# Kernel tuning notes

Measured on AMD Instinct MI355X. Metric: run time of the kernel, lower is better.

The kernel has to match this reference:

```python
import jax, jax.numpy as jnp
import numpy as np

PAD = 128  # attention_limit; window = 2*PAD+1 = 257


def setup_inputs() -> dict:
    key = jax.random.key(0)
    ks = jax.random.split(key, 8)
    B, S, E = 4, 4096, 512
    x = jax.random.normal(ks[0], (B, S, E), dtype=jnp.float32)
    mask = jax.random.randint(ks[1], (B, S, 1), 0, 2, dtype=jnp.int32)
    s = 1.0 / np.sqrt(E)
    Wq = jax.random.normal(ks[2], (E, E), dtype=jnp.float32) * s
    bq = jax.random.normal(ks[3], (E,), dtype=jnp.float32) * 0.01
    Wk = jax.random.normal(ks[4], (E, E), dtype=jnp.float32) * s
    bk = jax.random.normal(ks[5], (E,), dtype=jnp.float32) * 0.01
    Wv = jax.random.normal(ks[6], (E, E), dtype=jnp.float32) * s
    bv = jax.random.normal(ks[7], (E,), dtype=jnp.float32) * 0.01
    return {"x": x, "mask": mask, "Wq": Wq, "bq": bq, "Wk": Wk, "bk": bk, "Wv": Wv, "bv": bv}


def _local_attention(x, mask, Wq, bq, Wk, bk, Wv, bv):
    B, S, E = x.shape
    pad = PAD
    blk = pad                # block size = pad so window spans exactly 3 blocks
    nb = S // blk            # S chosen as a multiple of blk
    # Padded sequence: padded key/value positions get Linear(0)=bias and are
    # UNMASKED (original pads pre_mask with value=1) -- faithfully reproduced.
    ext = jnp.pad(x, ((0, 0), (pad, pad), (0, 0)))                    # [B,S+2p,E]
    pm = jnp.pad(mask.astype(jnp.float32), ((0, 0), (pad, pad), (0, 0)),
                 constant_values=1.0)[..., 0]                          # [B,S+2p]
    q = x @ Wq + bq                                                    # [B,S,E]
    k = ext @ Wk + bk                                                  # [B,S+2p,E]
    v = ext @ Wv + bv
    qb = q.reshape(B, nb, blk, E)
    kr = k.reshape(B, nb + 2, blk, E)
    vr = v.reshape(B, nb + 2, blk, E)
    pmr = pm.reshape(B, nb + 2, blk)
    # Query block b attends key blocks b, b+1, b+2 of the padded sequence.
    kb = jnp.concatenate([kr[:, i:i + nb] for i in range(3)], axis=2)   # [B,nb,3blk,E]
    vb = jnp.concatenate([vr[:, i:i + nb] for i in range(3)], axis=2)
    pmb = jnp.concatenate([pmr[:, i:i + nb] for i in range(3)], axis=2)  # [B,nb,3blk]
    e = jnp.einsum('bnqe,bnke->bnqk', qb, kb) / jnp.sqrt(jnp.float32(E))
    e = jnp.where(pmb[:, :, None, :] == 0, jnp.float32(-1e9), e)
    # Band mask: relative position d = k_idx - blk - q_idx must satisfy |d| <= pad;
    # out-of-band gets -inf so softmax matches the exact 257-wide window.
    qi = jnp.arange(blk)[:, None]
    ki = jnp.arange(3 * blk)[None, :]
    band = jnp.abs(ki - blk - qi) <= pad                                # [blk,3blk]
    e = jnp.where(band[None, None], e, -jnp.inf)
    a = jax.nn.softmax(e, axis=-1)                                      # [B,nb,blk,3blk]
    o = jnp.einsum('bnqk,bnke->bnqe', a, vb).reshape(B, S, E)
    return jnp.where(mask == 0, jnp.float32(0.0), o)


def reference(x, mask, Wq, bq, Wk, bk, Wv, bv):
    return _local_attention(x, mask, Wq, bq, Wk, bk, Wv, bv)
```

## Files before the change

kernel.cpp:

```cpp
#include <hip/hip_runtime.h>
#include <math.h>
#include <stdint.h>

#define BATCH 4
#define SEQ   4096
#define EMB   512
#define PADW  128
#define SPAD  (SEQ + 2*PADW)
#define WIN   (3*PADW)

static constexpr float SCALE = 0.04419417382415922f;

typedef __attribute__((ext_vector_type(8))) short    s16x8;
typedef __attribute__((ext_vector_type(4))) short    s16x4;
typedef __attribute__((ext_vector_type(4))) float    f32x4;
typedef __attribute__((ext_vector_type(8))) _Float16 f16x8;

__device__ __forceinline__ unsigned short f2h(float x) {
  _Float16 h = (_Float16)x;
  return __builtin_bit_cast(unsigned short, h);
}
__device__ __forceinline__ void gload16(const void* g, void* lds) {
  __builtin_amdgcn_global_load_lds(
      (const __attribute__((address_space(1))) uint32_t*)g,
      (__attribute__((address_space(3))) uint32_t*)lds, 16, 0, 0);
}
__device__ __forceinline__ f16x8 frag64(const unsigned short* base, int row, int slot) {
  return *(const f16x8*)((const char*)base + row * 128 + ((slot ^ (row & 7)) << 4));
}

__global__ __launch_bounds__(256) void convert_x(const float* __restrict__ x,
                                                 unsigned short* __restrict__ xh) {
  size_t i = ((size_t)blockIdx.x * 256 + threadIdx.x) * 8;
  float4 a = *(const float4*)&x[i];
  float4 c = *(const float4*)&x[i + 4];
  s16x8 o;
  o[0] = (short)f2h(a.x); o[1] = (short)f2h(a.y);
  o[2] = (short)f2h(a.z); o[3] = (short)f2h(a.w);
  o[4] = (short)f2h(c.x); o[5] = (short)f2h(c.y);
  o[6] = (short)f2h(c.z); o[7] = (short)f2h(c.w);
  *(s16x8*)&xh[i] = o;
}

__global__ __launch_bounds__(256) void convert_w(const float* __restrict__ Wq,
                                                 const float* __restrict__ Wk,
                                                 const float* __restrict__ Wv,
                                                 unsigned short* __restrict__ wt) {
  const int w = blockIdx.z;
  const float* W = (w == 0) ? Wq : (w == 1) ? Wk : Wv;
  const int kt = blockIdx.x * 64, nt = blockIdx.y * 64;
  __shared__ float T[64][65];
  const int tid = threadIdx.x;
  {
    int r = tid >> 4, c4 = (tid & 15) * 4;
#pragma unroll
    for (int i = 0; i < 4; ++i) {
      float4 v = *(const float4*)&W[(size_t)(kt + r + 16 * i) * EMB + nt + c4];
      T[r + 16 * i][c4 + 0] = v.x;
      T[r + 16 * i][c4 + 1] = v.y;
      T[r + 16 * i][c4 + 2] = v.z;
      T[r + 16 * i][c4 + 3] = v.w;
    }
  }
  __syncthreads();
  {
    int n = tid >> 2, k0 = (tid & 3) * 16;
    __align__(16) unsigned short hb[16];
#pragma unroll
    for (int j = 0; j < 16; ++j) hb[j] = f2h(T[k0 + j][n]);
    size_t base = ((size_t)w * EMB + nt + n) * EMB;
    *(s16x8*)&wt[base + kt + k0]     = *(s16x8*)&hb[0];
    *(s16x8*)&wt[base + kt + k0 + 8] = *(s16x8*)&hb[8];
  }
}

__global__ __launch_bounds__(256) void proj_kernel(
    const unsigned short* __restrict__ xh,
    const unsigned short* __restrict__ wt,
    const float* __restrict__ bq, const float* __restrict__ bk, const float* __restrict__ bv,
    unsigned short* __restrict__ qh,
    unsigned short* __restrict__ kh,
    unsigned short* __restrict__ vt)
{
  int linear = blockIdx.x + 34 * (blockIdx.y + 4 * blockIdx.z);
  linear = (linear & 7) * 204 + (linear >> 3);
  const int mt = linear % 34;
  const int nt = (linear / 34) & 3;
  const int z  = linear / 136;
  const int b = z / 3, w = z % 3;
  const float* bias = (w == 0) ? bq : (w == 1) ? bk : bv;
  const int tid = threadIdx.x, lane = tid & 63, wid = tid >> 6;
  const int t0 = mt * 128, n0 = nt * 128;

  if (mt == 0 || mt == 33) {
    if (w < 2) {
      unsigned short* om = (w == 0) ? qh : kh;
      for (int i = tid; i < 128 * 128; i += 256) {
        int r = i >> 7, n = i & 127;
        om[((size_t)b * SPAD + t0 + r) * EMB + n0 + n] = f2h(bias[n0 + n]);
      }
    } else {
      for (int i = tid; i < 128 * 128; i += 256) {
        int e = i >> 7, t = i & 127;
        vt[((size_t)b * EMB + n0 + e) * SPAD + t0 + t] = f2h(bias[n0 + e]);
      }
    }
    return;
  }

  __shared__ __align__(16) unsigned short smem[17408];
  unsigned short* At = smem;
  unsigned short* Bt = smem + 8192;

  f32x4 acc[4][4];
#pragma unroll
  for (int i = 0; i < 4; ++i)
#pragma unroll
    for (int j = 0; j < 4; ++j) acc[i][j] = (f32x4){0.f, 0.f, 0.f, 0.f};

  const int xr0 = (mt - 1) * 128;
  const int wm = wid >> 1, wn = wid & 1;

  for (int kt = 0; kt < EMB; kt += 64) {
#pragma unroll
    for (int i = 0; i < 4; ++i) {
      int c = wid * 256 + i * 64 + lane;
      int m = c >> 3, sl = (c & 7) ^ (m & 7);
      gload16(xh + ((size_t)b * SEQ + xr0 + m) * EMB + kt + sl * 8,
              (char*)At + (wid * 256 + i * 64) * 16);
    }
#pragma unroll
    for (int i = 0; i < 4; ++i) {
      int c = wid * 256 + i * 64 + lane;
      int n = c >> 3, sl = (c & 7) ^ (n & 7);
      gload16(wt + ((size_t)w * EMB + n0 + n) * EMB + kt + sl * 8,
              (char*)Bt + (wid * 256 + i * 64) * 16);
    }
    __syncthreads();
#pragma unroll
    for (int kk = 0; kk < 2; ++kk) {
      f16x8 af[4], bfr[4];
#pragma unroll
      for (int f = 0; f < 4; ++f)
        af[f] = frag64(At, wm * 64 + f * 16 + (lane & 15), kk * 4 + (lane >> 4));
#pragma unroll
      for (int f = 0; f < 4; ++f)
        bfr[f] = frag64(Bt, wn * 64 + f * 16 + (lane & 15), kk * 4 + (lane >> 4));
#pragma unroll
      for (int fm = 0; fm < 4; ++fm)
#pragma unroll
        for (int fn = 0; fn < 4; ++fn)
          acc[fm][fn] = __builtin_amdgcn_mfma_f32_16x16x32_f16(af[fm], bfr[fn], acc[fm][fn], 0, 0, 0);
    }
    __syncthreads();
  }

  if (w < 2) {
    unsigned short* om = (w == 0) ? qh : kh;
#pragma unroll
    for (int fm = 0; fm < 4; ++fm) {
      int t = t0 + wm * 64 + fm * 16 + ((lane >> 4) << 2);
#pragma unroll
      for (int fn = 0; fn < 4; ++fn) {
        int n = n0 + wn * 64 + fn * 16 + (lane & 15);
        float bsv = bias[n];
#pragma unroll
        for (int r = 0; r < 4; ++r)
          om[((size_t)b * SPAD + t + r) * EMB + n] = f2h(acc[fm][fn][r] + bsv);
      }
    }
  } else {
    unsigned short* T = smem;
#pragma unroll
    for (int fm = 0; fm < 4; ++fm) {
      int tl = wm * 64 + fm * 16 + ((lane >> 4) << 2);
#pragma unroll
      for (int fn = 0; fn < 4; ++fn) {
        int el = wn * 64 + fn * 16 + (lane & 15);
        float bsv = bias[n0 + el];
        s16x4 pk;
#pragma unroll
        for (int r = 0; r < 4; ++r) pk[r] = (short)f2h(acc[fm][fn][r] + bsv);
        *(s16x4*)&T[el * 136 + tl] = pk;
      }
    }
    __syncthreads();
#pragma unroll
    for (int it = 0; it < 8; ++it) {
      int c = it * 256 + tid;
      int e = c >> 4, t8 = (c & 15) * 8;
      s16x8 vchunk = *(s16x8*)&T[e * 136 + t8];
      *(s16x8*)&vt[((size_t)b * EMB + n0 + e) * SPAD + t0 + t8] = vchunk;
    }
  }
}

__global__ __launch_bounds__(512) void attn_kernel(
    const unsigned short* __restrict__ qh,
    const unsigned short* __restrict__ kh,
    const unsigned short* __restrict__ vt,
    const int* __restrict__ mask,
    float* __restrict__ out) {
  int linear = blockIdx.x + 64 * blockIdx.y;
  linear = (linear & 7) * 32 + (linear >> 3);
  const int b  = linear >> 6;
  const int s0 = (linear & 63) * 64;
  const int nb = s0 >> 7, o = s0 & 127;
  const int t0 = nb * 128;
  const int tid = threadIdx.x, lane = tid & 63, wid = tid >> 6;

  __shared__ __align__(16) char smem[88 * 1024];
  unsigned short* Kt = (unsigned short*)smem;
  unsigned short* Qt = (unsigned short*)(smem + 48 * 1024);
  float* red  = (float*)(smem + 48 * 1024);
  float* red2 = (float*)(smem + 48 * 1024 + 2048);
  float* invl = (float*)(smem + 48 * 1024 + 4096);
  float* Pm   = (float*)(smem + 48 * 1024 + 4352);
  unsigned short* Vt = (unsigned short*)(smem + 56 * 1024);

  f32x4 accS[3][4];
#pragma unroll
  for (int i = 0; i < 3; ++i)
#pragma unroll
    for (int j = 0; j < 4; ++j) accS[i][j] = (f32x4){0.f, 0.f, 0.f, 0.f};

  for (int kt = 0; kt < EMB; kt += 64) {
#pragma unroll
    for (int i = 0; i < 6; ++i) {
      int c = wid * 384 + i * 64 + lane;
      int r = c >> 3, sl = (c & 7) ^ (r & 7);
      gload16(kh + ((size_t)b * SPAD + t0 + r) * EMB + kt + sl * 8,
              (char*)Kt + (wid * 384 + i * 64) * 16);
    }
    {
      int c = wid * 64 + lane;
      int r = c >> 3, sl = (c & 7) ^ (r & 7);
      gload16(qh + ((size_t)b * SPAD + PADW + s0 + r) * EMB + kt + sl * 8,
              (char*)Qt + (wid * 64) * 16);
    }
    __syncthreads();
#pragma unroll
    for (int kk = 0; kk < 2; ++kk) {
      f16x8 af[3], bfq[4];
#pragma unroll
      for (int f = 0; f < 3; ++f)
        af[f] = frag64(Kt, wid * 48 + f * 16 + (lane & 15), kk * 4 + (lane >> 4));
#pragma unroll
      for (int f = 0; f < 4; ++f)
        bfq[f] = frag64(Qt, f * 16 + (lane & 15), kk * 4 + (lane >> 4));
#pragma unroll
      for (int fk = 0; fk < 3; ++fk)
#pragma unroll
        for (int fq = 0; fq < 4; ++fq)
          accS[fk][fq] = __builtin_amdgcn_mfma_f32_16x16x32_f16(af[fk], bfq[fq], accS[fk][fq], 0, 0, 0);
    }
    __syncthreads();
  }

  for (int k = tid; k < WIN; k += 512) {
    int t = t0 + k;
    Pm[k] = (t >= PADW && t < SEQ + PADW) ? (float)mask[(size_t)b * SEQ + (t - PADW)] : 1.f;
  }
  __syncthreads();

  float mx[4] = {-INFINITY, -INFINITY, -INFINITY, -INFINITY};
#pragma unroll
  for (int fk = 0; fk < 3; ++fk)
#pragma unroll
    for (int fq = 0; fq < 4; ++fq)
#pragma unroll
      for (int r = 0; r < 4; ++r) {
        int k = wid * 48 + fk * 16 + ((lane >> 4) << 2) + r;
        int p = o + fq * 16 + (lane & 15);
        float v;
        if (k < p || k > p + 2 * PADW) v = -INFINITY;
        else v = (Pm[k] == 0.f) ? -1e9f : accS[fk][fq][r] * SCALE;
        accS[fk][fq][r] = v;
        mx[fq] = fmaxf(mx[fq], v);
      }
#pragma unroll
  for (int fq = 0; fq < 4; ++fq) {
    mx[fq] = fmaxf(mx[fq], __shfl_xor(mx[fq], 16));
    mx[fq] = fmaxf(mx[fq], __shfl_xor(mx[fq], 32));
  }
  if (lane < 16) {
#pragma unroll
    for (int fq = 0; fq < 4; ++fq) red[wid * 64 + fq * 16 + lane] = mx[fq];
  }
  __syncthreads();
  float M[4];
#pragma unroll
  for (int fq = 0; fq < 4; ++fq) {
    float m = -INFINITY;
#pragma unroll
    for (int ww = 0; ww < 8; ++ww) m = fmaxf(m, red[ww * 64 + fq * 16 + (lane & 15)]);
    M[fq] = m;
  }
  float sm[4] = {0.f, 0.f, 0.f, 0.f};
#pragma unroll
  for (int fk = 0; fk < 3; ++fk)
#pragma unroll
    for (int fq = 0; fq < 4; ++fq)
#pragma unroll
      for (int r = 0; r < 4; ++r) {
        float pv = __expf(accS[fk][fq][r] - M[fq]);
        accS[fk][fq][r] = pv;
        sm[fq] += pv;
      }
#pragma unroll
  for (int fq = 0; fq < 4; ++fq) {
    sm[fq] += __shfl_xor(sm[fq], 16);
    sm[fq] += __shfl_xor(sm[fq], 32);
  }
  if (lane < 16) {
#pragma unroll
    for (int fq = 0; fq < 4; ++fq) red2[wid * 64 + fq * 16 + lane] = sm[fq];
  }
  __syncthreads();
  {
    float L[4];
#pragma unroll
    for (int fq = 0; fq < 4; ++fq) {
      float s = 0.f;
#pragma unroll
      for (int ww = 0; ww < 8; ++ww) s += red2[ww * 64 + fq * 16 + (lane & 15)];
      L[fq] = s;
    }
    if (wid == 0 && lane < 16) {
#pragma unroll
      for (int fq = 0; fq < 4; ++fq) invl[fq * 16 + lane] = 1.f / L[fq];
    }
  }
#pragma unroll
  for (int fk = 0; fk < 3; ++fk)
#pragma unroll
    for (int fq = 0; fq < 4; ++fq) {
      int k0 = wid * 48 + fk * 16 + ((lane >> 4) << 2);
      int q = fq * 16 + (lane & 15);
      s16x4 pk;
      pk[0] = (short)f2h(accS[fk][fq][0]);
      pk[1] = (short)f2h(accS[fk][fq][1]);
      pk[2] = (short)f2h(accS[fk][fq][2]);
      pk[3] = (short)f2h(accS[fk][fq][3]);
      int sl = k0 >> 3;
      *(s16x4*)((char*)Kt + q * 768 + (((sl ^ (q & 7))) << 4) + ((k0 & 7) << 1)) = pk;
    }
  __syncthreads();

  f32x4 accO[4][4];
#pragma unroll
  for (int i = 0; i < 4; ++i)
#pragma unroll
    for (int j = 0; j < 4; ++j) accO[i][j] = (f32x4){0.f, 0.f, 0.f, 0.f};

  for (int kb = 0; kb < WIN; kb += 32) {
#pragma unroll
    for (int i = 0; i < 4; ++i) {
      int c = wid * 256 + i * 64 + lane;
      int e = c >> 2, sl = (c & 3) ^ (e & 3);
      gload16(vt + ((size_t)b * EMB + e) * SPAD + t0 + kb + sl * 8,
              (char*)Vt + (wid * 256 + i * 64) * 16);
    }
    __syncthreads();
    f16x8 pa[4], vb[4];
#pragma unroll
    for (int fq = 0; fq < 4; ++fq) {
      int q = fq * 16 + (lane & 15);
      int sl = (kb + ((lane >> 4) << 3)) >> 3;
      pa[fq] = *(const f16x8*)((const char*)Kt + q * 768 + ((sl ^ (q & 7)) << 4));
    }
#pragma unroll
    for (int fe = 0; fe < 4; ++fe) {
      int e = wid * 64 + fe * 16 + (lane & 15);
      int sl = (lane >> 4) ^ (e & 3);
      vb[fe] = *(const f16x8*)((const char*)Vt + e * 64 + (sl << 4));
    }
#pragma unroll
    for (int fq = 0; fq < 4; ++fq)
#pragma unroll
      for (int fe = 0; fe < 4; ++fe)
        accO[fq][fe] = __builtin_amdgcn_mfma_f32_16x16x32_f16(pa[fq], vb[fe], accO[fq][fe], 0, 0, 0);
    __syncthreads();
  }

#pragma unroll
  for (int fq = 0; fq < 4; ++fq)
#pragma unroll
    for (int r = 0; r < 4; ++r) {
      int q = fq * 16 + ((lane >> 4) << 2) + r;
      float sc = invl[q] * ((Pm[PADW + o + q] != 0.f) ? 1.f : 0.f);
#pragma unroll
      for (int fe = 0; fe < 4; ++fe) {
        int e = wid * 64 + fe * 16 + (lane & 15);
        out[((size_t)b * SEQ + s0 + q) * EMB + e] = accO[fq][fe][r] * sc;
      }
    }
}

extern "C" void kernel_launch(void* const* d_in, const int* in_sizes, int n_in,
                              void* d_out, int out_size, void* d_ws, size_t ws_size,
                              hipStream_t stream) {
  const float* x  = (const float*)d_in[0];
  const int* mask = (const int*)d_in[1];
  const float* Wq = (const float*)d_in[2];
  const float* bq = (const float*)d_in[3];
  const float* Wk = (const float*)d_in[4];
  const float* bk = (const float*)d_in[5];
  const float* Wv = (const float*)d_in[6];
  const float* bv = (const float*)d_in[7];
  float* out = (float*)d_out;

  char* ws = (char*)d_ws;
  unsigned short* xh = (unsigned short*)ws;
  unsigned short* wt = (unsigned short*)(ws + 16777216);
  unsigned short* qh = (unsigned short*)(ws + 18350080);
  unsigned short* kh = (unsigned short*)(ws + 36175872);
  unsigned short* vt = (unsigned short*)(ws + 54001664);

  convert_x<<<dim3(4096), 256, 0, stream>>>(x, xh);
  convert_w<<<dim3(8, 8, 3), 256, 0, stream>>>(Wq, Wk, Wv, wt);
  proj_kernel<<<dim3(34, 4, 12), 256, 0, stream>>>(xh, wt, bq, bk, bv, qh, kh, vt);
  attn_kernel<<<dim3(SEQ / 64, BATCH), 512, 0, stream>>>(qh, kh, vt, mask, out);
}
```

Baseline: 174.5 us.

## Load Q/K/V fragments directly from global memory and skip out-of-band key tiles

The attention kernel no longer stages K, Q and V through LDS with global_load_lds and per-step barriers. Each wave now reads its MFMA fragments straight from global memory. Waves whose 48-key slice lies outside the query band skip the QK^T GEMM, and the PV loop covers only the 320 keys that can be non-zero. Mask values are read into registers instead of an LDS table, LDS use shrinks to about 52KB, and launch bounds request 4 blocks per SM. The projection kernel's block-index swizzle is also reordered. In exchange, reuse across waves now depends on L1/L2 caching, and the direct global reads may be uncoalesced.

```diff
diff --git a/kernel.cpp b/kernel.cpp
--- a/kernel.cpp
+++ b/kernel.cpp
@@ -83,11 +83,13 @@
     unsigned short* __restrict__ vt)
 {
   int linear = blockIdx.x + 34 * (blockIdx.y + 4 * blockIdx.z);
-  linear = (linear & 7) * 204 + (linear >> 3);
-  const int mt = linear % 34;
-  const int nt = (linear / 34) & 3;
-  const int z  = linear / 136;
-  const int b = z / 3, w = z % 3;
+  int swz = (linear & 7) * 204 + (linear >> 3);
+  const int w  = swz % 3;
+  int rest = swz / 3;
+  const int mt = rest % 34;
+  rest /= 34;
+  const int nt = rest & 3;
+  const int b  = rest >> 2;
   const float* bias = (w == 0) ? bq : (w == 1) ? bk : bv;
   const int tid = threadIdx.x, lane = tid & 63, wid = tid >> 6;
   const int t0 = mt * 128, n0 = nt * 128;
@@ -195,7 +197,7 @@
   }
 }
 
-__global__ __launch_bounds__(512) void attn_kernel(
+__global__ __launch_bounds__(512, 4) void attn_kernel(
     const unsigned short* __restrict__ qh,
     const unsigned short* __restrict__ kh,
     const unsigned short* __restrict__ vt,
@@ -209,14 +211,15 @@
   const int t0 = nb * 128;
   const int tid = threadIdx.x, lane = tid & 63, wid = tid >> 6;
 
-  __shared__ __align__(16) char smem[88 * 1024];
-  unsigned short* Kt = (unsigned short*)smem;
-  unsigned short* Qt = (unsigned short*)(smem + 48 * 1024);
-  float* red  = (float*)(smem + 48 * 1024);
-  float* red2 = (float*)(smem + 48 * 1024 + 2048);
-  float* invl = (float*)(smem + 48 * 1024 + 4096);
-  float* Pm   = (float*)(smem + 48 * 1024 + 4352);
-  unsigned short* Vt = (unsigned short*)(smem + 56 * 1024);
+  __shared__ __align__(16) char smem[53504];
+  unsigned short* P = (unsigned short*)smem;
+  float* red  = (float*)(smem + 49152);
+  float* red2 = (float*)(smem + 51200);
+  float* invl = (float*)(smem + 53248);
+
+  const int l15 = lane & 15;
+  const int oct = (lane >> 4) << 3;
+  const int kr0 = wid * 48;
 
   f32x4 accS[3][4];
 #pragma unroll
@@ -224,44 +227,37 @@
 #pragma unroll
     for (int j = 0; j < 4; ++j) accS[i][j] = (f32x4){0.f, 0.f, 0.f, 0.f};
 
-  for (int kt = 0; kt < EMB; kt += 64) {
-#pragma unroll
-    for (int i = 0; i < 6; ++i) {
-      int c = wid * 384 + i * 64 + lane;
-      int r = c >> 3, sl = (c & 7) ^ (r & 7);
-      gload16(kh + ((size_t)b * SPAD + t0 + r) * EMB + kt + sl * 8,
-              (char*)Kt + (wid * 384 + i * 64) * 16);
-    }
-    {
-      int c = wid * 64 + lane;
-      int r = c >> 3, sl = (c & 7) ^ (r & 7);
-      gload16(qh + ((size_t)b * SPAD + PADW + s0 + r) * EMB + kt + sl * 8,
-              (char*)Qt + (wid * 64) * 16);
-    }
-    __syncthreads();
-#pragma unroll
-    for (int kk = 0; kk < 2; ++kk) {
+  const bool active = (kr0 < o + 320) && (kr0 + 48 > o);
+  if (active) {
+    const unsigned short* kp = kh + ((size_t)b * SPAD + t0 + kr0 + l15) * EMB;
+    const unsigned short* qp = qh + ((size_t)b * SPAD + PADW + s0 + l15) * EMB;
+#pragma unroll 4
+    for (int kt = 0; kt < EMB; kt += 32) {
       f16x8 af[3], bfq[4];
 #pragma unroll
       for (int f = 0; f < 3; ++f)
-        af[f] = frag64(Kt, wid * 48 + f * 16 + (lane & 15), kk * 4 + (lane >> 4));
+        af[f] = *(const f16x8*)&kp[(size_t)f * 16 * EMB + kt + oct];
 #pragma unroll
       for (int f = 0; f < 4; ++f)
-        bfq[f] = frag64(Qt, f * 16 + (lane & 15), kk * 4 + (lane >> 4));
+        bfq[f] = *(const f16x8*)&qp[(size_t)f * 16 * EMB + kt + oct];
 #pragma unroll
       for (int fk = 0; fk < 3; ++fk)
 #pragma unroll
         for (int fq = 0; fq < 4; ++fq)
           accS[fk][fq] = __builtin_amdgcn_mfma_f32_16x16x32_f16(af[fk], bfq[fq], accS[fk][fq], 0, 0, 0);
     }
-    __syncthreads();
-  }
-
-  for (int k = tid; k < WIN; k += 512) {
-    int t = t0 + k;
-    Pm[k] = (t >= PADW && t < SEQ + PADW) ? (float)mask[(size_t)b * SEQ + (t - PADW)] : 1.f;
-  }
-  __syncthreads();
+  }
+
+  float pmv[3][4];
+#pragma unroll
+  for (int fk = 0; fk < 3; ++fk) {
+    int kq = kr0 + fk * 16 + ((lane >> 4) << 2);
+    int tq = t0 + kq - PADW;
+    int4 mv = make_int4(1, 1, 1, 1);
+    if (tq >= 0 && tq < SEQ) mv = *(const int4*)&mask[(size_t)b * SEQ + tq];
+    pmv[fk][0] = (float)mv.x; pmv[fk][1] = (float)mv.y;
+    pmv[fk][2] = (float)mv.z; pmv[fk][3] = (float)mv.w;
+  }
 
   float mx[4] = {-INFINITY, -INFINITY, -INFINITY, -INFINITY};
 #pragma unroll
@@ -270,11 +266,11 @@
     for (int fq = 0; fq < 4; ++fq)
 #pragma unroll
       for (int r = 0; r < 4; ++r) {
-        int k = wid * 48 + fk * 16 + ((lane >> 4) << 2) + r;
-        int p = o + fq * 16 + (lane & 15);
+        int k = kr0 + fk * 16 + ((lane >> 4) << 2) + r;
+        int p = o + fq * 16 + l15;
         float v;
         if (k < p || k > p + 2 * PADW) v = -INFINITY;
-        else v = (Pm[k] == 0.f) ? -1e9f : accS[fk][fq][r] * SCALE;
+        else v = (pmv[fk][r] == 0.f) ? -1e9f : accS[fk][fq][r] * SCALE;
         accS[fk][fq][r] = v;
         mx[fq] = fmaxf(mx[fq], v);
       }
@@ -293,7 +289,7 @@
   for (int fq = 0; fq < 4; ++fq) {
     float m = -INFINITY;
 #pragma unroll
-    for (int ww = 0; ww < 8; ++ww) m = fmaxf(m, red[ww * 64 + fq * 16 + (lane & 15)]);
+    for (int ww = 0; ww < 8; ++ww) m = fmaxf(m, red[ww * 64 + fq * 16 + l15]);
     M[fq] = m;
   }
   float sm[4] = {0.f, 0.f, 0.f, 0.f};
@@ -317,33 +313,28 @@
     for (int fq = 0; fq < 4; ++fq) red2[wid * 64 + fq * 16 + lane] = sm[fq];
   }
   __syncthreads();
-  {
-    float L[4];
+  if (wid == 0 && lane < 16) {
 #pragma unroll
     for (int fq = 0; fq < 4; ++fq) {
       float s = 0.f;
 #pragma unroll
-      for (int ww = 0; ww < 8; ++ww) s += red2[ww * 64 + fq * 16 + (lane & 15)];
-      L[fq] = s;
-    }
-    if (wid == 0 && lane < 16) {
-#pragma unroll
-      for (int fq = 0; fq < 4; ++fq) invl[fq * 16 + lane] = 1.f / L[fq];
+      for (int ww = 0; ww < 8; ++ww) s += red2[ww * 64 + fq * 16 + lane];
+      invl[fq * 16 + lane] = 1.f / s;
     }
   }
 #pragma unroll
   for (int fk = 0; fk < 3; ++fk)
 #pragma unroll
     for (int fq = 0; fq < 4; ++fq) {
-      int k0 = wid * 48 + fk * 16 + ((lane >> 4) << 2);
-      int q = fq * 16 + (lane & 15);
+      int k0 = kr0 + fk * 16 + ((lane >> 4) << 2);
+      int q = fq * 16 + l15;
       s16x4 pk;
       pk[0] = (short)f2h(accS[fk][fq][0]);
       pk[1] = (short)f2h(accS[fk][fq][1]);
       pk[2] = (short)f2h(accS[fk][fq][2]);
       pk[3] = (short)f2h(accS[fk][fq][3]);
       int sl = k0 >> 3;
-      *(s16x4*)((char*)Kt + q * 768 + (((sl ^ (q & 7))) << 4) + ((k0 & 7) << 1)) = pk;
+      *(s16x4*)((char*)P + q * 768 + ((sl ^ (q & 7)) << 4) + ((k0 & 7) << 1)) = pk;
     }
   __syncthreads();
 
@@ -353,48 +344,42 @@
 #pragma unroll
     for (int j = 0; j < 4; ++j) accO[i][j] = (f32x4){0.f, 0.f, 0.f, 0.f};
 
-  for (int kb = 0; kb < WIN; kb += 32) {
-#pragma unroll
-    for (int i = 0; i < 4; ++i) {
-      int c = wid * 256 + i * 64 + lane;
-      int e = c >> 2, sl = (c & 3) ^ (e & 3);
-      gload16(vt + ((size_t)b * EMB + e) * SPAD + t0 + kb + sl * 8,
-              (char*)Vt + (wid * 256 + i * 64) * 16);
-    }
-    __syncthreads();
+  const unsigned short* vp = vt + ((size_t)b * EMB + wid * 64 + l15) * SPAD + t0;
+#pragma unroll 2
+  for (int kb = o; kb < o + 320; kb += 32) {
     f16x8 pa[4], vb[4];
 #pragma unroll
     for (int fq = 0; fq < 4; ++fq) {
-      int q = fq * 16 + (lane & 15);
-      int sl = (kb + ((lane >> 4) << 3)) >> 3;
-      pa[fq] = *(const f16x8*)((const char*)Kt + q * 768 + ((sl ^ (q & 7)) << 4));
-    }
-#pragma unroll
-    for (int fe = 0; fe < 4; ++fe) {
-      int e = wid * 64 + fe * 16 + (lane & 15);
-      int sl = (lane >> 4) ^ (e & 3);
-      vb[fe] = *(const f16x8*)((const char*)Vt + e * 64 + (sl << 4));
-    }
+      int q = fq * 16 + l15;
+      int sl = (kb >> 3) + (lane >> 4);
+      pa[fq] = *(const f16x8*)((const char*)P + q * 768 + ((sl ^ (q & 7)) << 4));
+    }
+#pragma unroll
+    for (int fe = 0; fe < 4; ++fe)
+      vb[fe] = *(const f16x8*)&vp[(size_t)fe * 16 * SPAD + kb + oct];
 #pragma unroll
     for (int fq = 0; fq < 4; ++fq)
 #pragma unroll
       for (int fe = 0; fe < 4; ++fe)
         accO[fq][fe] = __builtin_amdgcn_mfma_f32_16x16x32_f16(pa[fq], vb[fe], accO[fq][fe], 0, 0, 0);
-    __syncthreads();
-  }
-
-#pragma unroll
-  for (int fq = 0; fq < 4; ++fq)
+  }
+
+#pragma unroll
+  for (int fq = 0; fq < 4; ++fq) {
+    int qq = fq * 16 + ((lane >> 4) << 2);
+    int4 mq4 = *(const int4*)&mask[(size_t)b * SEQ + s0 + qq];
+    int mqa[4] = {mq4.x, mq4.y, mq4.z, mq4.w};
 #pragma unroll
     for (int r = 0; r < 4; ++r) {
-      int q = fq * 16 + ((lane >> 4) << 2) + r;
-      float sc = invl[q] * ((Pm[PADW + o + q] != 0.f) ? 1.f : 0.f);
+      int q = qq + r;
+      float sc = invl[q] * ((mqa[r] != 0) ? 1.f : 0.f);
 #pragma unroll
       for (int fe = 0; fe < 4; ++fe) {
-        int e = wid * 64 + fe * 16 + (lane & 15);
+        int e = wid * 64 + fe * 16 + l15;
         out[((size_t)b * SEQ + s0 + q) * EMB + e] = accO[fq][fe][r] * sc;
       }
     }
+  }
 }
 
 extern "C" void kernel_launch(void* const* d_in, const int* in_sizes, int n_in,
```

Measured after the change: 180.7 us. +3.5%, slower.
